# Kernel optimization log

Hardware: AMD Instinct MI355X
Metric: run time of the kernel (lower is better)

## Reference

```python
import jax, jax.numpy as jnp
import numpy as np

NUM_HEADS = 16
NUM_HIDDENS = 1024
D_K = NUM_HIDDENS // NUM_HEADS
NEG_INF = -1.0e9


def setup_inputs() -> dict:
    key = jax.random.key(0)
    kx, kq, kk, kv, ko, kl = jax.random.split(key, 6)
    B, S, D = 2, 2048, NUM_HIDDENS
    scale = 1.0 / np.sqrt(D)
    return {
        "X": jax.random.normal(kx, (B, S, D), dtype=jnp.float32),
        "valid_lens": jax.random.randint(kl, (B,), 0, S, dtype=jnp.int64),
        "W_q": jax.random.normal(kq, (D, D), dtype=jnp.float32) * scale,
        "W_k": jax.random.normal(kk, (D, D), dtype=jnp.float32) * scale,
        "W_v": jax.random.normal(kv, (D, D), dtype=jnp.float32) * scale,
        "W_o": jax.random.normal(ko, (D, D), dtype=jnp.float32) * scale,
    }


def _split_heads(x):
    # [B, S, D] -> [B, H, S, d_k]
    B, S, _ = x.shape
    return x.reshape(B, S, NUM_HEADS, D_K).transpose(0, 2, 1, 3)


def reference(X, valid_lens, W_q, W_k, W_v, W_o):
    B, S, D = X.shape
    # nn.Linear(bias=False): y = x @ W.T  (W is [out, in])
    Q = _split_heads(jnp.einsum("bsd,ed->bse", X, W_q))  # [B,H,S,dk]
    K = _split_heads(jnp.einsum("bsd,ed->bse", X, W_k))
    V = _split_heads(jnp.einsum("bsd,ed->bse", X, W_v))

    scores = jnp.einsum("bhqd,bhkd->bhqk", Q, K) / jnp.sqrt(
        jnp.asarray(D_K, dtype=X.dtype)
    )  # [B,H,S,S]

    # key-position mask per batch: positions >= valid_len get -1e9
    mask = jnp.arange(S)[None, :] >= valid_lens[:, None]  # [B,S]
    scores = jnp.where(mask[:, None, None, :], jnp.asarray(NEG_INF, X.dtype), scores)

    attn = jax.nn.softmax(scores, axis=-1)  # dropout p=0 -> identity
    out = jnp.einsum("bhqk,bhkd->bhqd", attn, V)  # [B,H,S,dk]
    out = out.transpose(0, 2, 1, 3).reshape(B, S, D)
    return jnp.einsum("bsd,ed->bse", out, W_o)
```

## Files before the change

### kernel.cpp

```cpp
#include <hip/hip_runtime.h>
#include <stdint.h>

#define S_LEN 2048
#define BATCH 2
#define DMODEL 1024
#define NHEAD 16
#define DK 64
#define MROWS (BATCH * S_LEN)

typedef __attribute__((ext_vector_type(8))) short bf16x8;
typedef __attribute__((ext_vector_type(4))) float f32x4;
typedef __attribute__((ext_vector_type(4))) short short4v;

__device__ __forceinline__ short f2b(float f) {
    union { float f; uint32_t u; } c; c.f = f;
    uint32_t u = c.u;
    return (short)((u + 0x7fffu + ((u >> 16) & 1u)) >> 16);
}

__device__ __forceinline__ void gload16(const void* g, void* l) {
    __builtin_amdgcn_global_load_lds(
        (const __attribute__((address_space(1))) void*)g,
        (__attribute__((address_space(3))) void*)l, 16, 0, 0);
}

__global__ void cvt_kernel(const float* __restrict__ X, const float* __restrict__ Wq,
                           const float* __restrict__ Wk, const float* __restrict__ Wv,
                           const float* __restrict__ Wo,
                           short* __restrict__ Xb, short* __restrict__ Wqb,
                           short* __restrict__ Wkb, short* __restrict__ Wvb,
                           short* __restrict__ Wob) {
    const float* src; short* dst; int n4;
    switch (blockIdx.y) {
        case 0:  src = X;  dst = Xb;  n4 = MROWS * DMODEL / 4;  break;
        case 1:  src = Wq; dst = Wqb; n4 = DMODEL * DMODEL / 4; break;
        case 2:  src = Wk; dst = Wkb; n4 = DMODEL * DMODEL / 4; break;
        case 3:  src = Wv; dst = Wvb; n4 = DMODEL * DMODEL / 4; break;
        default: src = Wo; dst = Wob; n4 = DMODEL * DMODEL / 4; break;
    }
    for (int i = blockIdx.x * blockDim.x + threadIdx.x; i < n4;
         i += gridDim.x * blockDim.x) {
        float4 v = ((const float4*)src)[i];
        short4v o;
        o[0] = f2b(v.x); o[1] = f2b(v.y); o[2] = f2b(v.z); o[3] = f2b(v.w);
        ((short4v*)dst)[i] = o;
    }
}

template <int OUT_F32>
__global__ __launch_bounds__(256) void gemm_bt(
    const short* __restrict__ A,
    const short* __restrict__ Bt0, const short* __restrict__ Bt1,
    const short* __restrict__ Bt2,
    short* __restrict__ Cb0, short* __restrict__ Cb1, short* __restrict__ Cb2,
    float* __restrict__ Cf, int M, int N, int K) {
    __shared__ short sA[128 * 32];
    __shared__ short sB[128 * 32];

    const short* Bt = Bt0;
    short* Cb = Cb0;
    if (blockIdx.z == 1) { Bt = Bt1; Cb = Cb1; }
    else if (blockIdx.z == 2) { Bt = Bt2; Cb = Cb2; }

    const int tid = threadIdx.x;
    const int lane = tid & 63;
    const int wid = tid >> 6;
    const int wr = wid >> 1, wc = wid & 1;
    const int brow = blockIdx.y * 128;
    const int bcol = blockIdx.x * 128;
    const int lr = lane & 15;
    const int kh = (lane >> 4) << 3;

    f32x4 acc[4][4] = {};

    const int idx0 = tid, idx1 = tid + 256;
    const int ar0 = idx0 >> 2, ak0 = (idx0 & 3) << 3;
    const int ar1 = idx1 >> 2, ak1 = (idx1 & 3) << 3;

    const int nk = K >> 5;
    for (int kt = 0; kt < nk; ++kt) {
        __syncthreads();
        const int k0 = kt << 5;
        gload16(A + (size_t)(brow + ar0) * K + k0 + ak0, &sA[idx0 * 8]);
        gload16(A + (size_t)(brow + ar1) * K + k0 + ak1, &sA[idx1 * 8]);
        gload16(Bt + (size_t)(bcol + ar0) * K + k0 + ak0, &sB[idx0 * 8]);
        gload16(Bt + (size_t)(bcol + ar1) * K + k0 + ak1, &sB[idx1 * 8]);
        __syncthreads();

        bf16x8 a[4], b[4];
#pragma unroll
        for (int mt = 0; mt < 4; ++mt)
            a[mt] = *(const bf16x8*)&sA[(wr * 64 + mt * 16 + lr) * 32 + kh];
#pragma unroll
        for (int nt = 0; nt < 4; ++nt)
            b[nt] = *(const bf16x8*)&sB[(wc * 64 + nt * 16 + lr) * 32 + kh];
#pragma unroll
        for (int mt = 0; mt < 4; ++mt)
#pragma unroll
            for (int nt = 0; nt < 4; ++nt)
                acc[mt][nt] = __builtin_amdgcn_mfma_f32_16x16x32_bf16(
                    a[mt], b[nt], acc[mt][nt], 0, 0, 0);
    }

    const int rbase = (lane >> 4) << 2;
    const bool vtrans = (!OUT_F32) && (blockIdx.z == 2);
#pragma unroll
    for (int mt = 0; mt < 4; ++mt) {
#pragma unroll
        for (int nt = 0; nt < 4; ++nt) {
            if (vtrans) {
                int row0 = brow + wr * 64 + mt * 16 + rbase;
                int col = bcol + wc * 64 + nt * 16 + lr;
                int bb = row0 >> 11, key = row0 & 2047;
                int hh = col >> 6, d = col & 63;
                short4v pk;
#pragma unroll
                for (int j = 0; j < 4; ++j) pk[j] = f2b(acc[mt][nt][j]);
                *(short4v*)&Cb[((size_t)((bb * 16 + hh) * 64 + d)) * S_LEN + key] = pk;
            } else {
#pragma unroll
                for (int j = 0; j < 4; ++j) {
                    int row = brow + wr * 64 + mt * 16 + rbase + j;
                    int col = bcol + wc * 64 + nt * 16 + lr;
                    if (OUT_F32)
                        Cf[(size_t)row * N + col] = acc[mt][nt][j];
                    else
                        Cb[(size_t)row * N + col] = f2b(acc[mt][nt][j]);
                }
            }
        }
    }
}

__global__ __launch_bounds__(256) void attn_kernel(
    const short* __restrict__ Q, const short* __restrict__ K,
    const short* __restrict__ Vt, short* __restrict__ O,
    const int* __restrict__ vlens) {
    __shared__ short sK[2][64 * 64];
    __shared__ short sV[2][64 * 64];
    __shared__ short sP[4][16 * 64];

    const int tid = threadIdx.x;
    const int lane = tid & 63;
    const int w = tid >> 6;
    const int id = blockIdx.x;
    const int id2 = ((id & 7) << 7) | (id >> 3);
    const int qb = id2 & 31;
    const int bhx = id2 >> 5;
    const int b = bhx & 1, h = bhx >> 1;
    const int lr = lane & 15;
    const int kh = (lane >> 4) << 3;
    const int rbase = (lane >> 4) << 2;
    const int swq = (lr & 7) << 3;

    int vl = vlens[b];
    if (vl < 0) vl = 0;
    if (vl > S_LEN) vl = S_LEN;
    const bool allm = (vl == 0);
    if (allm) vl = S_LEN;
    const int nT = (vl + 63) >> 6;
    const int nFull = ((vl & 63) == 0) ? nT : nT - 1;

    const size_t rowbase = (size_t)(b * S_LEN) * DMODEL + h * DK;
    const short* vt = Vt + ((size_t)((b * 16 + h) * 64)) * S_LEN;

    const short* qrow = Q + rowbase + (size_t)(qb * 64 + w * 16 + lr) * DMODEL;
    bf16x8 qf0 = *(const bf16x8*)(qrow + kh);
    bf16x8 qf1 = *(const bf16x8*)(qrow + 32 + kh);
    if (allm) {
#pragma unroll
        for (int i = 0; i < 8; ++i) { qf0[i] = 0; qf1[i] = 0; }
    }

    f32x4 oac[4] = {};
    float m_run = -1e30f, l_run = 0.f;
    const float CEXP = 0.18033688011112042f;

    const int kr0 = tid >> 3;
    const int kr1 = kr0 + 32;
    const int kc0 = (((tid & 7) ^ (kr0 & 7)) << 3);
    const int kc1 = (((tid & 7) ^ (kr1 & 7)) << 3);

    uint32_t* sPw = (uint32_t*)&sP[w][0];

    {
        const short* kbase = K + rowbase;
        gload16(kbase + (size_t)kr0 * DMODEL + kc0, &sK[0][tid * 8]);
        gload16(kbase + (size_t)kr1 * DMODEL + kc1, &sK[0][(tid + 256) * 8]);
        gload16(vt + (size_t)kr0 * S_LEN + kc0, &sV[0][tid * 8]);
        gload16(vt + (size_t)kr1 * S_LEN + kc1, &sV[0][(tid + 256) * 8]);
    }
    __syncthreads();

#define TILE_BODY(MASKED_C)                                                     \
    do {                                                                        \
        constexpr bool MASKED = MASKED_C;                                       \
        const short* sKc = sK[cur];                                             \
        const short* sVc = sV[cur];                                             \
        f32x4 sacc[4] = {};                                                     \
        __builtin_amdgcn_s_setprio(1);                                          \
        _Pragma("unroll")                                                       \
        for (int nt = 0; nt < 4; ++nt) {                                        \
            int R = nt * 16 + lr;                                               \
            int sw = (R & 7) << 3;                                              \
            bf16x8 kb0 = *(const bf16x8*)&sKc[R * 64 + (kh ^ sw)];              \
            bf16x8 kb1 = *(const bf16x8*)&sKc[R * 64 + ((32 + kh) ^ sw)];       \
            sacc[nt] = __builtin_amdgcn_mfma_f32_16x16x32_bf16(                 \
                kb0, qf0, sacc[nt], 0, 0, 0);                                   \
            sacc[nt] = __builtin_amdgcn_mfma_f32_16x16x32_bf16(                 \
                kb1, qf1, sacc[nt], 0, 0, 0);                                   \
        }                                                                       \
        __builtin_amdgcn_s_setprio(0);                                          \
        float s[16];                                                            \
        _Pragma("unroll")                                                       \
        for (int nt = 0; nt < 4; ++nt)                                          \
            _Pragma("unroll")                                                   \
            for (int j = 0; j < 4; ++j) {                                       \
                float v = sacc[nt][j];                                          \
                if (MASKED) {                                                   \
                    int keyi = t * 64 + nt * 16 + rbase + j;                    \
                    if (keyi >= vl) v = -3.0e38f;                               \
                }                                                               \
                s[nt * 4 + j] = v;                                              \
            }                                                                   \
        float mx01 = fmaxf(fmaxf(s[0], s[1]), fmaxf(s[2], s[3]));               \
        float mx23 = fmaxf(fmaxf(s[4], s[5]), fmaxf(s[6], s[7]));               \
        float mx45 = fmaxf(fmaxf(s[8], s[9]), fmaxf(s[10], s[11]));             \
        float mx67 = fmaxf(fmaxf(s[12], s[13]), fmaxf(s[14], s[15]));           \
        float mx = fmaxf(fmaxf(mx01, mx23), fmaxf(mx45, mx67));                 \
        mx = fmaxf(mx, __shfl_xor(mx, 16));                                     \
        mx = fmaxf(mx, __shfl_xor(mx, 32));                                     \
        float mnew = fmaxf(m_run, mx);                                          \
        float mc = mnew * CEXP;                                                 \
        float scl = __builtin_exp2f(m_run * CEXP - mc);                         \
        float p[16];                                                            \
        _Pragma("unroll")                                                       \
        for (int i = 0; i < 16; ++i)                                            \
            p[i] = __builtin_exp2f(s[i] * CEXP - mc);                           \
        float ls = ((p[0] + p[1]) + (p[2] + p[3])) +                            \
                   ((p[4] + p[5]) + (p[6] + p[7]));                             \
        ls += ((p[8] + p[9]) + (p[10] + p[11])) +                               \
              ((p[12] + p[13]) + (p[14] + p[15]));                              \
        ls += __shfl_xor(ls, 16);                                               \
        ls += __shfl_xor(ls, 32);                                               \
        l_run = l_run * scl + ls;                                               \
        m_run = mnew;                                                           \
        _Pragma("unroll")                                                       \
        for (int nt = 0; nt < 4; ++nt)                                          \
            _Pragma("unroll")                                                   \
            for (int pi = 0; pi < 2; ++pi) {                                    \
                uint32_t r;                                                     \
                asm("v_cvt_pk_bf16_f32 %0, %1, %2"                              \
                    : "=v"(r)                                                   \
                    : "v"(p[nt * 4 + 2 * pi]), "v"(p[nt * 4 + 2 * pi + 1]));    \
                int key0 = nt * 16 + rbase + 2 * pi;                            \
                sPw[(lr * 64 + (key0 ^ swq)) >> 1] = r;                         \
            }                                                                   \
        float sclq[4];                                                          \
        _Pragma("unroll")                                                       \
        for (int j = 0; j < 4; ++j) sclq[j] = __shfl(scl, rbase + j);           \
        _Pragma("unroll")                                                       \
        for (int dt = 0; dt < 4; ++dt)                                          \
            _Pragma("unroll")                                                   \
            for (int j = 0; j < 4; ++j) oac[dt][j] *= sclq[j];                  \
        __builtin_amdgcn_s_setprio(1);                                          \
        _Pragma("unroll")                                                       \
        for (int ks = 0; ks < 2; ++ks) {                                        \
            bf16x8 pf = *(const bf16x8*)&sP[w][lr * 64 + ((ks * 32 + kh) ^ swq)]; \
            _Pragma("unroll")                                                   \
            for (int dt = 0; dt < 4; ++dt) {                                    \
                int drow = dt * 16 + lr;                                        \
                int swv = (drow & 7) << 3;                                      \
                bf16x8 vf = *(const bf16x8*)&sVc[drow * 64 +                    \
                                                 ((ks * 32 + kh) ^ swv)];       \
                oac[dt] = __builtin_amdgcn_mfma_f32_16x16x32_bf16(              \
                    pf, vf, oac[dt], 0, 0, 0);                                  \
            }                                                                   \
        }                                                                       \
        __builtin_amdgcn_s_setprio(0);                                          \
    } while (0)

    int cur = 0;
    for (int t = 0; t < nT; ++t) {
        const bool hn = (t + 1 < nT);
        if (hn) {
            short* sKn = sK[cur ^ 1];
            short* sVn = sV[cur ^ 1];
            const short* kbase = K + rowbase + (size_t)((t + 1) * 64) * DMODEL;
            gload16(kbase + (size_t)kr0 * DMODEL + kc0, &sKn[tid * 8]);
            gload16(kbase + (size_t)kr1 * DMODEL + kc1, &sKn[(tid + 256) * 8]);
            const short* vbase = vt + (t + 1) * 64;
            gload16(vbase + (size_t)kr0 * S_LEN + kc0, &sVn[tid * 8]);
            gload16(vbase + (size_t)kr1 * S_LEN + kc1, &sVn[(tid + 256) * 8]);
        }

        if (t < nFull) TILE_BODY(false);
        else TILE_BODY(true);

        __syncthreads();
        cur ^= 1;
    }
#undef TILE_BODY

    float rl = 1.f / l_run;
    float rlq[4];
#pragma unroll
    for (int j = 0; j < 4; ++j) rlq[j] = __shfl(rl, rbase + j);
#pragma unroll
    for (int dt = 0; dt < 4; ++dt) {
#pragma unroll
        for (int j = 0; j < 4; ++j) {
            int q = qb * 64 + w * 16 + rbase + j;
            O[rowbase + (size_t)q * DMODEL + dt * 16 + lr] = f2b(oac[dt][j] * rlq[j]);
        }
    }
}

extern "C" void kernel_launch(void* const* d_in, const int* in_sizes, int n_in,
                              void* d_out, int out_size, void* d_ws, size_t ws_size,
                              hipStream_t stream) {
    const float* X = (const float*)d_in[0];
    const int* vlens = (const int*)d_in[1];
    const float* Wq = (const float*)d_in[2];
    const float* Wk = (const float*)d_in[3];
    const float* Wv = (const float*)d_in[4];
    const float* Wo = (const float*)d_in[5];
    float* out = (float*)d_out;

    short* Xb = (short*)d_ws;
    short* Wqb = Xb + (size_t)MROWS * DMODEL;
    short* Wkb = Wqb + (size_t)DMODEL * DMODEL;
    short* Wvb = Wkb + (size_t)DMODEL * DMODEL;
    short* Wob = Wvb + (size_t)DMODEL * DMODEL;
    short* Qb = Wob + (size_t)DMODEL * DMODEL;
    short* Kb = Qb + (size_t)MROWS * DMODEL;
    short* Vtb = Kb + (size_t)MROWS * DMODEL;
    short* Ob = Vtb + (size_t)MROWS * DMODEL;

    cvt_kernel<<<dim3(512, 5), 256, 0, stream>>>(X, Wq, Wk, Wv, Wo, Xb, Wqb, Wkb,
                                                 Wvb, Wob);
    gemm_bt<0><<<dim3(8, 32, 3), 256, 0, stream>>>(Xb, Wqb, Wkb, Wvb, Qb, Kb, Vtb,
                                                   nullptr, MROWS, DMODEL, DMODEL);
    attn_kernel<<<dim3(1024), 256, 0, stream>>>(Qb, Kb, Vtb, Ob, vlens);
    gemm_bt<1><<<dim3(8, 32, 1), 256, 0, stream>>>(Ob, Wob, Wob, Wob, nullptr,
                                                   nullptr, nullptr, out, MROWS,
                                                   DMODEL, DMODEL);
}
```

Measured before the change: 117.8 us.

## Use lazy max rescaling and transposed PV MFMA in flash attention

The running max and the O/l rescale are now updated only when a tile max exceeds the current max by a threshold. This skips the cross-lane max/sum reductions and the per-tile rescale in the common case. The PV MFMA operands are swapped so each lane holds its own query's accumulator, which removes the scale broadcast shuffles and allows a vectorized output store. P is written to LDS in 8-byte chunks, LDS/global addresses are precomputed, and the row-sum reduction is deferred to the epilogue. The lazy threshold risks precision loss or overflow if scores grow within the threshold window.

```diff
diff --git a/kernel.cpp b/kernel.cpp
--- a/kernel.cpp
+++ b/kernel.cpp
@@ -11,6 +11,7 @@
 typedef __attribute__((ext_vector_type(8))) short bf16x8;
 typedef __attribute__((ext_vector_type(4))) float f32x4;
 typedef __attribute__((ext_vector_type(4))) short short4v;
+typedef __attribute__((ext_vector_type(2))) uint32_t u32x2;
 
 __device__ __forceinline__ short f2b(float f) {
     union { float f; uint32_t u; } c; c.f = f;
@@ -173,23 +174,27 @@
     }
 
     f32x4 oac[4] = {};
-    float m_run = -1e30f, l_run = 0.f;
+    float m_run = -1e30f, m_c = -1e30f, l_run = 0.f;
     const float CEXP = 0.18033688011112042f;
+    const float THRADD = 44.361419556f;
+
+    const int lofs0 = lr * 64 + (kh ^ swq);
+    const int lofs1 = lr * 64 + ((32 + kh) ^ swq);
 
     const int kr0 = tid >> 3;
     const int kr1 = kr0 + 32;
     const int kc0 = (((tid & 7) ^ (kr0 & 7)) << 3);
     const int kc1 = (((tid & 7) ^ (kr1 & 7)) << 3);
 
-    uint32_t* sPw = (uint32_t*)&sP[w][0];
-
-    {
-        const short* kbase = K + rowbase;
-        gload16(kbase + (size_t)kr0 * DMODEL + kc0, &sK[0][tid * 8]);
-        gload16(kbase + (size_t)kr1 * DMODEL + kc1, &sK[0][(tid + 256) * 8]);
-        gload16(vt + (size_t)kr0 * S_LEN + kc0, &sV[0][tid * 8]);
-        gload16(vt + (size_t)kr1 * S_LEN + kc1, &sV[0][(tid + 256) * 8]);
-    }
+    const short* kA = K + rowbase + (size_t)kr0 * DMODEL + kc0;
+    const short* kB = K + rowbase + (size_t)kr1 * DMODEL + kc1;
+    const short* vA = vt + (size_t)kr0 * S_LEN + kc0;
+    const short* vB = vt + (size_t)kr1 * S_LEN + kc1;
+
+    gload16(kA, &sK[0][tid * 8]);
+    gload16(kB, &sK[0][(tid + 256) * 8]);
+    gload16(vA, &sV[0][tid * 8]);
+    gload16(vB, &sV[0][(tid + 256) * 8]);
     __syncthreads();
 
 #define TILE_BODY(MASKED_C)                                                     \
@@ -197,84 +202,89 @@
         constexpr bool MASKED = MASKED_C;                                       \
         const short* sKc = sK[cur];                                             \
         const short* sVc = sV[cur];                                             \
+        const short* kL0 = sKc + lofs0;                                         \
+        const short* kL1 = sKc + lofs1;                                         \
         f32x4 sacc[4] = {};                                                     \
         __builtin_amdgcn_s_setprio(1);                                          \
         _Pragma("unroll")                                                       \
         for (int nt = 0; nt < 4; ++nt) {                                        \
-            int R = nt * 16 + lr;                                               \
-            int sw = (R & 7) << 3;                                              \
-            bf16x8 kb0 = *(const bf16x8*)&sKc[R * 64 + (kh ^ sw)];              \
-            bf16x8 kb1 = *(const bf16x8*)&sKc[R * 64 + ((32 + kh) ^ sw)];       \
+            bf16x8 kb0 = *(const bf16x8*)&kL0[nt * 1024];                       \
+            bf16x8 kb1 = *(const bf16x8*)&kL1[nt * 1024];                       \
             sacc[nt] = __builtin_amdgcn_mfma_f32_16x16x32_bf16(                 \
                 kb0, qf0, sacc[nt], 0, 0, 0);                                   \
             sacc[nt] = __builtin_amdgcn_mfma_f32_16x16x32_bf16(                 \
                 kb1, qf1, sacc[nt], 0, 0, 0);                                   \
         }                                                                       \
         __builtin_amdgcn_s_setprio(0);                                          \
-        float s[16];                                                            \
+        if (MASKED) {                                                           \
+            _Pragma("unroll")                                                   \
+            for (int nt = 0; nt < 4; ++nt)                                      \
+                _Pragma("unroll")                                               \
+                for (int j = 0; j < 4; ++j) {                                   \
+                    int keyi = t * 64 + nt * 16 + rbase + j;                    \
+                    if (keyi >= vl) sacc[nt][j] = -3.0e38f;                     \
+                }                                                               \
+        }                                                                       \
+        float t0 = fmaxf(fmaxf(sacc[0][0], sacc[0][1]), sacc[0][2]);            \
+        float t1 = fmaxf(fmaxf(sacc[0][3], sacc[1][0]), sacc[1][1]);            \
+        float t2 = fmaxf(fmaxf(sacc[1][2], sacc[1][3]), sacc[2][0]);            \
+        float t3 = fmaxf(fmaxf(sacc[2][1], sacc[2][2]), sacc[2][3]);            \
+        float t4 = fmaxf(fmaxf(sacc[3][0], sacc[3][1]), sacc[3][2]);            \
+        float pmax = fmaxf(fmaxf(fmaxf(t0, t1), t2),                            \
+                           fmaxf(fmaxf(t3, t4), sacc[3][3]));                   \
+        if (__any(pmax > m_run + THRADD)) {                                     \
+            float mx = pmax;                                                    \
+            mx = fmaxf(mx, __shfl_xor(mx, 16));                                 \
+            mx = fmaxf(mx, __shfl_xor(mx, 32));                                 \
+            float scl = __builtin_exp2f((m_run - mx) * CEXP);                   \
+            m_run = mx;                                                         \
+            m_c = mx * CEXP;                                                    \
+            l_run *= scl;                                                       \
+            _Pragma("unroll")                                                   \
+            for (int dt = 0; dt < 4; ++dt)                                      \
+                _Pragma("unroll")                                               \
+                for (int j = 0; j < 4; ++j) oac[dt][j] *= scl;                  \
+        }                                                                       \
+        float p[16];                                                            \
         _Pragma("unroll")                                                       \
         for (int nt = 0; nt < 4; ++nt)                                          \
             _Pragma("unroll")                                                   \
-            for (int j = 0; j < 4; ++j) {                                       \
-                float v = sacc[nt][j];                                          \
-                if (MASKED) {                                                   \
-                    int keyi = t * 64 + nt * 16 + rbase + j;                    \
-                    if (keyi >= vl) v = -3.0e38f;                               \
-                }                                                               \
-                s[nt * 4 + j] = v;                                              \
-            }                                                                   \
-        float mx01 = fmaxf(fmaxf(s[0], s[1]), fmaxf(s[2], s[3]));               \
-        float mx23 = fmaxf(fmaxf(s[4], s[5]), fmaxf(s[6], s[7]));               \
-        float mx45 = fmaxf(fmaxf(s[8], s[9]), fmaxf(s[10], s[11]));             \
-        float mx67 = fmaxf(fmaxf(s[12], s[13]), fmaxf(s[14], s[15]));           \
-        float mx = fmaxf(fmaxf(mx01, mx23), fmaxf(mx45, mx67));                 \
-        mx = fmaxf(mx, __shfl_xor(mx, 16));                                     \
-        mx = fmaxf(mx, __shfl_xor(mx, 32));                                     \
-        float mnew = fmaxf(m_run, mx);                                          \
-        float mc = mnew * CEXP;                                                 \
-        float scl = __builtin_exp2f(m_run * CEXP - mc);                         \
-        float p[16];                                                            \
-        _Pragma("unroll")                                                       \
-        for (int i = 0; i < 16; ++i)                                            \
-            p[i] = __builtin_exp2f(s[i] * CEXP - mc);                           \
+            for (int j = 0; j < 4; ++j)                                         \
+                p[nt * 4 + j] = __builtin_exp2f(                                \
+                    __builtin_fmaf(sacc[nt][j], CEXP, -m_c));                   \
         float ls = ((p[0] + p[1]) + (p[2] + p[3])) +                            \
                    ((p[4] + p[5]) + (p[6] + p[7]));                             \
         ls += ((p[8] + p[9]) + (p[10] + p[11])) +                               \
               ((p[12] + p[13]) + (p[14] + p[15]));                              \
-        ls += __shfl_xor(ls, 16);                                               \
-        ls += __shfl_xor(ls, 32);                                               \
-        l_run = l_run * scl + ls;                                               \
-        m_run = mnew;                                                           \
+        l_run += ls;                                                            \
         _Pragma("unroll")                                                       \
-        for (int nt = 0; nt < 4; ++nt)                                          \
-            _Pragma("unroll")                                                   \
-            for (int pi = 0; pi < 2; ++pi) {                                    \
-                uint32_t r;                                                     \
-                asm("v_cvt_pk_bf16_f32 %0, %1, %2"                              \
-                    : "=v"(r)                                                   \
-                    : "v"(p[nt * 4 + 2 * pi]), "v"(p[nt * 4 + 2 * pi + 1]));    \
-                int key0 = nt * 16 + rbase + 2 * pi;                            \
-                sPw[(lr * 64 + (key0 ^ swq)) >> 1] = r;                         \
+        for (int nt = 0; nt < 4; ++nt) {                                        \
+            u32x2 r;                                                            \
+            asm("v_cvt_pk_bf16_f32 %0, %1, %2"                                  \
+                : "=v"(r[0]) : "v"(p[nt * 4 + 0]), "v"(p[nt * 4 + 1]));         \
+            asm("v_cvt_pk_bf16_f32 %0, %1, %2"                                  \
+                : "=v"(r[1]) : "v"(p[nt * 4 + 2]), "v"(p[nt * 4 + 3]));         \
+            *(u32x2*)&sP[w][lr * 64 + ((nt * 16 + rbase) ^ swq)] = r;           \
+        }                                                                       \
+        const short* pL0 = &sP[w][lofs0];                                       \
+        const short* pL1 = &sP[w][lofs1];                                       \
+        const short* vL0 = sVc + lofs0;                                         \
+        const short* vL1 = sVc + lofs1;                                         \
+        __builtin_amdgcn_s_setprio(1);                                          \
+        {                                                                       \
+            bf16x8 pf0 = *(const bf16x8*)pL0;                                   \
+            _Pragma("unroll")                                                   \
+            for (int dt = 0; dt < 4; ++dt) {                                    \
+                bf16x8 vf = *(const bf16x8*)&vL0[dt * 1024];                    \
+                oac[dt] = __builtin_amdgcn_mfma_f32_16x16x32_bf16(              \
+                    vf, pf0, oac[dt], 0, 0, 0);                                 \
             }                                                                   \
-        float sclq[4];                                                          \
-        _Pragma("unroll")                                                       \
-        for (int j = 0; j < 4; ++j) sclq[j] = __shfl(scl, rbase + j);           \
-        _Pragma("unroll")                                                       \
-        for (int dt = 0; dt < 4; ++dt)                                          \
-            _Pragma("unroll")                                                   \
-            for (int j = 0; j < 4; ++j) oac[dt][j] *= sclq[j];                  \
-        __builtin_amdgcn_s_setprio(1);                                          \
-        _Pragma("unroll")                                                       \
-        for (int ks = 0; ks < 2; ++ks) {                                        \
-            bf16x8 pf = *(const bf16x8*)&sP[w][lr * 64 + ((ks * 32 + kh) ^ swq)]; \
+            bf16x8 pf1 = *(const bf16x8*)pL1;                                   \
             _Pragma("unroll")                                                   \
             for (int dt = 0; dt < 4; ++dt) {                                    \
-                int drow = dt * 16 + lr;                                        \
-                int swv = (drow & 7) << 3;                                      \
-                bf16x8 vf = *(const bf16x8*)&sVc[drow * 64 +                    \
-                                                 ((ks * 32 + kh) ^ swv)];       \
+                bf16x8 vf = *(const bf16x8*)&vL1[dt * 1024];                    \
                 oac[dt] = __builtin_amdgcn_mfma_f32_16x16x32_bf16(              \
-                    pf, vf, oac[dt], 0, 0, 0);                                  \
+                    vf, pf1, oac[dt], 0, 0, 0);                                 \
             }                                                                   \
         }                                                                       \
         __builtin_amdgcn_s_setprio(0);                                          \
@@ -286,12 +296,12 @@
         if (hn) {
             short* sKn = sK[cur ^ 1];
             short* sVn = sV[cur ^ 1];
-            const short* kbase = K + rowbase + (size_t)((t + 1) * 64) * DMODEL;
-            gload16(kbase + (size_t)kr0 * DMODEL + kc0, &sKn[tid * 8]);
-            gload16(kbase + (size_t)kr1 * DMODEL + kc1, &sKn[(tid + 256) * 8]);
-            const short* vbase = vt + (t + 1) * 64;
-            gload16(vbase + (size_t)kr0 * S_LEN + kc0, &sVn[tid * 8]);
-            gload16(vbase + (size_t)kr1 * S_LEN + kc1, &sVn[(tid + 256) * 8]);
+            kA += 64 * DMODEL; kB += 64 * DMODEL;
+            vA += 64; vB += 64;
+            gload16(kA, &sKn[tid * 8]);
+            gload16(kB, &sKn[(tid + 256) * 8]);
+            gload16(vA, &sVn[tid * 8]);
+            gload16(vB, &sVn[(tid + 256) * 8]);
         }
 
         if (t < nFull) TILE_BODY(false);
@@ -302,17 +312,17 @@
     }
 #undef TILE_BODY
 
-    float rl = 1.f / l_run;
-    float rlq[4];
-#pragma unroll
-    for (int j = 0; j < 4; ++j) rlq[j] = __shfl(rl, rbase + j);
+    float lt = l_run + __shfl_xor(l_run, 16);
+    lt += __shfl_xor(lt, 32);
+    float rl = 1.f / lt;
+
+    short* orow = O + rowbase + (size_t)(qb * 64 + w * 16 + lr) * DMODEL;
 #pragma unroll
     for (int dt = 0; dt < 4; ++dt) {
-#pragma unroll
-        for (int j = 0; j < 4; ++j) {
-            int q = qb * 64 + w * 16 + rbase + j;
-            O[rowbase + (size_t)q * DMODEL + dt * 16 + lr] = f2b(oac[dt][j] * rlq[j]);
-        }
+        short4v pk;
+#pragma unroll
+        for (int j = 0; j < 4; ++j) pk[j] = f2b(oac[dt][j] * rl);
+        *(short4v*)&orow[dt * 16 + rbase] = pk;
     }
 }
 
```

New measurement: 119.7 us. About the same (+1.6%).
